# Kernel optimization log

Measured on AMD Instinct MI355X. Metric: run time of the kernel, lower is better.

Reference implementation:

```python
import jax, jax.numpy as jnp
import numpy as np

B, R, NB, T = 32, 96, 5, 2048
FEAT_DIM = 64
SPARSITY = 0.2


def _per_band(X, community, W1, b1, W2, b2):
    # X: [R, T] wavelet coeffs for one (batch, band) slice
    n, t = X.shape
    f32 = X.dtype
    # --- functional connectivity (cosine of centered signals == Pearson corr) ---
    Xc = X - X.mean(axis=1, keepdims=True)
    norm = jnp.linalg.norm(Xc, axis=1, keepdims=True)
    norm = jnp.where(norm == 0, 1.0, norm)
    C = (Xc @ Xc.T) / (norm * norm.T)
    C = jnp.nan_to_num(C, nan=0.0)
    C = C * (1.0 - jnp.eye(n, dtype=f32))  # zero diagonal
    # --- quantile sparsification over strict lower triangle ---
    ti, tj = np.tril_indices(n, -1)
    thr = jnp.quantile(jnp.abs(C[ti, tj]), 1.0 - SPARSITY)
    A = C * (jnp.abs(C) >= thr).astype(f32)  # graph_type == 'weighted'
    # --- node features (5-dim, averaged over regions) ---
    mean_f = X.mean(axis=1)
    std_f = jnp.std(X, axis=1, ddof=1)  # torch.std is unbiased
    energy_f = (X ** 2).sum(axis=1)
    maxamp_f = jnp.abs(X).max(axis=1)
    ps = jnp.abs(jnp.fft.fft(X, axis=1)) ** 2
    ps = ps[:, : t // 2]
    s = ps.sum(axis=1, keepdims=True)
    s = jnp.where(s == 0, 1.0, s)
    p = ps / s
    ent_f = -(p * jnp.log(p + 1e-10)).sum(axis=1)
    node5 = jnp.stack([mean_f, std_f, energy_f, maxamp_f, ent_f], axis=1).mean(axis=0)
    # --- graph properties (6-dim) on binarized adjacency ---
    Bm = (A != 0).astype(f32)
    ne = Bm.sum() / 2.0
    density = ne / (n * (n - 1) / 2.0)
    deg = Bm.sum(axis=1)
    avg_deg = deg.mean()
    A2 = Bm @ Bm
    tri = (A2 * Bm).sum() / 6.0
    poss = (deg * (deg - 1.0)).sum() / 2.0
    clus = jnp.where(poss > 0, tri / jnp.where(poss > 0, poss, 1.0), 0.0)
    # global efficiency: safe reciprocal (zero where A+I == 0; original would emit inf)
    denom = Bm + jnp.eye(n, dtype=f32)
    eff = jnp.where(denom > 0, 1.0 / jnp.where(denom > 0, denom, 1.0), 0.0).sum() / (n * (n - 1))
    # approximate modularity with fixed 2-community assignment (deterministic)
    m2 = 2.0 * ne
    m2_safe = jnp.where(m2 > 0, m2, 1.0)
    same = (community[:, None] == community[None, :]) & (~jnp.eye(n, dtype=bool))
    expected = jnp.outer(deg, deg) / m2_safe
    mod = jnp.where(m2 > 0, (same * (Bm - expected)).sum() / m2_safe, 0.0)
    props = jnp.stack([ne, density, avg_deg, clus, eff, mod])
    feat11 = jnp.concatenate([node5, props])  # [11]
    # --- feature encoder MLP (dropout is identity at inference) ---
    h = jnp.maximum(feat11 @ W1.T + b1, 0.0)
    return A, h @ W2.T + b2


def _forward(wavelet_coeffs, frequency_bands, community, W1, b1, W2, b2):
    b, r, nb, t = wavelet_coeffs.shape
    Xs = wavelet_coeffs.transpose(0, 2, 1, 3).reshape(b * nb, r, t)  # [B*NB, R, T]
    A, F = jax.vmap(_per_band, in_axes=(0, None, None, None, None, None))(
        Xs, community, W1, b1, W2, b2)
    return A.reshape(b, nb, r, r), F.reshape(b, nb, -1)


def setup_inputs() -> dict:
    key = jax.random.key(0)
    k0, k1, k2, k3, k4 = jax.random.split(key, 5)
    wavelet_coeffs = jax.random.normal(k0, (B, R, NB, T), dtype=jnp.float32)
    frequency_bands = jax.random.uniform(k1, (NB, 2), dtype=jnp.float32)
    community = jax.random.randint(k2, (R,), 0, 2)
    W1 = jax.random.normal(k3, (32, 11), dtype=jnp.float32) * 0.3
    b1 = jnp.zeros((32,), jnp.float32)
    W2 = jax.random.normal(k4, (FEAT_DIM, 32), dtype=jnp.float32) * 0.18
    b2 = jnp.zeros((FEAT_DIM,), jnp.float32)
    return {"wavelet_coeffs": wavelet_coeffs, "frequency_bands": frequency_bands,
            "community": community, "W1": W1, "b1": b1, "W2": W2, "b2": b2}


def reference(wavelet_coeffs, frequency_bands, community, W1, b1, W2, b2):
    return _forward(wavelet_coeffs, frequency_bands, community, W1, b1, W2, b2)
```

## Files before the change

kernel.cpp:

```cpp
#include <hip/hip_runtime.h>
#include <hip/hip_bf16.h>
#include <math.h>
#include <float.h>

#ifndef M_PI
#define M_PI 3.14159265358979323846
#endif

#define NBANDS 160
#define RR 96
#define TT 2048
#define NTRIL 4560
#define A_ELEMS ((size_t)NBANDS * RR * RR)
#define NBIN 16384
#define MAXCAND 512

#define KS 8
#define CHUNK 256
#define BKS 64
#define GPITCH 72

#define PHI(L) ((L) ^ (((L) >> 5) & 31))

typedef float  f32x4  __attribute__((ext_vector_type(4)));
typedef __bf16 bf16x8 __attribute__((ext_vector_type(8)));
typedef __bf16 bf16x4 __attribute__((ext_vector_type(4)));

__device__ inline void blockReduceSum4(double v0, double v1, double v2, double v3,
                                       double* sred, double out[4]) {
    for (int off = 32; off > 0; off >>= 1) {
        v0 += __shfl_down(v0, off, 64);
        v1 += __shfl_down(v1, off, 64);
        v2 += __shfl_down(v2, off, 64);
        v3 += __shfl_down(v3, off, 64);
    }
    int lane = threadIdx.x & 63, wid = threadIdx.x >> 6;
    if (lane == 0) {
        sred[wid * 4 + 0] = v0; sred[wid * 4 + 1] = v1;
        sred[wid * 4 + 2] = v2; sred[wid * 4 + 3] = v3;
    }
    __syncthreads();
    if (threadIdx.x < 4) {
        double r = sred[threadIdx.x] + sred[4 + threadIdx.x]
                 + sred[8 + threadIdx.x] + sred[12 + threadIdx.x];
        sred[16 + threadIdx.x] = r;
    }
    __syncthreads();
    out[0] = sred[16]; out[1] = sred[17]; out[2] = sred[18]; out[3] = sred[19];
    __syncthreads();
}

__device__ inline void blockReduceSum2(double v0, double v1,
                                       double* sred, double out[2]) {
    for (int off = 32; off > 0; off >>= 1) {
        v0 += __shfl_down(v0, off, 64);
        v1 += __shfl_down(v1, off, 64);
    }
    int lane = threadIdx.x & 63, wid = threadIdx.x >> 6;
    if (lane == 0) { sred[wid * 2 + 0] = v0; sred[wid * 2 + 1] = v1; }
    __syncthreads();
    if (threadIdx.x < 2) {
        double r = sred[threadIdx.x] + sred[2 + threadIdx.x]
                 + sred[4 + threadIdx.x] + sred[6 + threadIdx.x];
        sred[8 + threadIdx.x] = r;
    }
    __syncthreads();
    out[0] = sred[8]; out[1] = sred[9];
    __syncthreads();
}

__device__ inline void blockReduceMax4(double v0, double v1, double v2, double v3,
                                       double* sred, double out[4]) {
    for (int off = 32; off > 0; off >>= 1) {
        v0 = fmax(v0, __shfl_down(v0, off, 64));
        v1 = fmax(v1, __shfl_down(v1, off, 64));
        v2 = fmax(v2, __shfl_down(v2, off, 64));
        v3 = fmax(v3, __shfl_down(v3, off, 64));
    }
    int lane = threadIdx.x & 63, wid = threadIdx.x >> 6;
    if (lane == 0) {
        sred[wid * 4 + 0] = v0; sred[wid * 4 + 1] = v1;
        sred[wid * 4 + 2] = v2; sred[wid * 4 + 3] = v3;
    }
    __syncthreads();
    if (threadIdx.x < 4) {
        double r = fmax(fmax(sred[threadIdx.x], sred[4 + threadIdx.x]),
                        fmax(sred[8 + threadIdx.x], sred[12 + threadIdx.x]));
        sred[16 + threadIdx.x] = r;
    }
    __syncthreads();
    out[0] = sred[16]; out[1] = sred[17]; out[2] = sred[18]; out[3] = sred[19];
    __syncthreads();
}

__global__ void twiddle_kernel(float* tw) {
    int k = blockIdx.x * blockDim.x + threadIdx.x;
    if (k < 1024) {
        double ang = -2.0 * M_PI * (double)k / 2048.0;
        tw[2 * k]     = (float)cos(ang);
        tw[2 * k + 1] = (float)sin(ang);
    }
}

#define BFLYD(r1, r2, WR, WI) do { \
    float _wr = (WR), _wi = (WI); \
    float _t1r = _wr * yr1[r2] - _wi * yi1[r2]; \
    float _t1i = _wr * yi1[r2] + _wi * yr1[r2]; \
    yr1[r2] = yr1[r1] - _t1r; yi1[r2] = yi1[r1] - _t1i; \
    yr1[r1] += _t1r; yi1[r1] += _t1i; \
    float _t2r = _wr * yr2[r2] - _wi * yi2[r2]; \
    float _t2i = _wr * yi2[r2] + _wi * yr2[r2]; \
    yr2[r2] = yr2[r1] - _t2r; yi2[r2] = yi2[r1] - _t2i; \
    yr2[r1] += _t2r; yi2[r1] += _t2i; } while (0)

__global__ __launch_bounds__(256) void rowstat_fft_kernel(
    const float* __restrict__ wc, const float* __restrict__ tw,
    double* __restrict__ rowstats)
{
    __shared__ float re1[TT];
    __shared__ float im1[TT];
    __shared__ float re2[TT];
    __shared__ float im2[TT];
    __shared__ double sred[24];
    __shared__ double statout[12];
    __shared__ float bcast[8];

    int t = threadIdx.x;
    int g0 = blockIdx.x * 4;

    int band = g0 / RR, r0 = g0 % RR;
    int b = band / 5, nb = band % 5;
    size_t base0 = ((size_t)(b * RR + r0) * 5 + nb) * TT;
    const size_t RSTR = (size_t)5 * TT;
    const float2* twv = (const float2*)tw;

    float s0 = 0.f, s1 = 0.f, s2 = 0.f, s3 = 0.f;
    float q0 = 0.f, q1 = 0.f, q2 = 0.f, q3 = 0.f;
    float m0 = 0.f, m1 = 0.f, m2 = 0.f, m3 = 0.f;
#pragma unroll
    for (int c = 0; c < 8; c++) {
        int i = t + c * 256;
        float a0 = wc[base0 + i];
        float a1 = wc[base0 + RSTR + i];
        float a2 = wc[base0 + 2 * RSTR + i];
        float a3 = wc[base0 + 3 * RSTR + i];
        int P = PHI(i);
        re1[P] = a0; im1[P] = a1; re2[P] = a2; im2[P] = a3;
        s0 += a0; s1 += a1; s2 += a2; s3 += a3;
        q0 = fmaf(a0, a0, q0); q1 = fmaf(a1, a1, q1);
        q2 = fmaf(a2, a2, q2); q3 = fmaf(a3, a3, q3);
        m0 = fmaxf(m0, fabsf(a0)); m1 = fmaxf(m1, fabsf(a1));
        m2 = fmaxf(m2, fabsf(a2)); m3 = fmaxf(m3, fabsf(a3));
    }
    __syncthreads();

    {
        double S[4], Q[4], M[4];
        blockReduceSum4((double)s0, (double)s1, (double)s2, (double)s3, sred, S);
        blockReduceSum4((double)q0, (double)q1, (double)q2, (double)q3, sred, Q);
        blockReduceMax4((double)m0, (double)m1, (double)m2, (double)m3, sred, M);
        if (t == 0) {
            statout[0] = S[0]; statout[1] = S[1]; statout[2] = S[2]; statout[3] = S[3];
            statout[4] = Q[0]; statout[5] = Q[1]; statout[6] = Q[2]; statout[7] = Q[3];
            statout[8] = M[0]; statout[9] = M[1]; statout[10] = M[2]; statout[11] = M[3];
        }
    }

    float yr1[8], yi1[8], yr2[8], yi2[8];

#pragma unroll
    for (int j = 0; j < 8; j++) {
        int p = 8 * t + j;
        int L = (int)(__brev((unsigned)p) >> 21);
        int P = PHI(L);
        yr1[j] = re1[P]; yi1[j] = im1[P];
        yr2[j] = re2[P]; yi2[j] = im2[P];
    }

    const float RC = 0.70710678f;
    BFLYD(0, 1, 1.0f, 0.0f); BFLYD(2, 3, 1.0f, 0.0f);
    BFLYD(4, 5, 1.0f, 0.0f); BFLYD(6, 7, 1.0f, 0.0f);
    BFLYD(0, 2, 1.0f, 0.0f); BFLYD(1, 3, 0.0f, -1.0f);
    BFLYD(4, 6, 1.0f, 0.0f); BFLYD(5, 7, 0.0f, -1.0f);
    BFLYD(0, 4, 1.0f, 0.0f); BFLYD(1, 5, RC, -RC);
    BFLYD(2, 6, 0.0f, -1.0f); BFLYD(3, 7, -RC, -RC);

    __syncthreads();
#pragma unroll
    for (int j = 0; j < 8; j++) {
        int P = PHI(8 * t + j);
        re1[P] = yr1[j]; im1[P] = yi1[j];
        re2[P] = yr2[j]; im2[P] = yi2[j];
    }
    __syncthreads();
    int oo = t & 7;
    int bb64 = 4 * ((t >> 3) & 7) + (t >> 6);
#pragma unroll
    for (int k = 0; k < 8; k++) {
        int P = PHI(64 * bb64 + 8 * k + oo);
        yr1[k] = re1[P]; yi1[k] = im1[P];
        yr2[k] = re2[P]; yi2[k] = im2[P];
    }

    {
        float2 w0 = twv[oo << 7];
        BFLYD(0, 1, w0.x, w0.y); BFLYD(2, 3, w0.x, w0.y);
        BFLYD(4, 5, w0.x, w0.y); BFLYD(6, 7, w0.x, w0.y);
        float2 wa = twv[oo << 6];
        float2 wb = twv[(oo + 8) << 6];
        BFLYD(0, 2, wa.x, wa.y); BFLYD(1, 3, wb.x, wb.y);
        BFLYD(4, 6, wa.x, wa.y); BFLYD(5, 7, wb.x, wb.y);
        float2 wc0 = twv[oo << 5], wc1 = twv[(oo + 8) << 5];
        float2 wc2 = twv[(oo + 16) << 5], wc3 = twv[(oo + 24) << 5];
        BFLYD(0, 4, wc0.x, wc0.y);
        BFLYD(1, 5, wc1.x, wc1.y);
        BFLYD(2, 6, wc2.x, wc2.y);
        BFLYD(3, 7, wc3.x, wc3.y);
    }

    __syncthreads();
#pragma unroll
    for (int k = 0; k < 8; k++) {
        int P = PHI(64 * bb64 + 8 * k + oo);
        re1[P] = yr1[k]; im1[P] = yi1[k];
        re2[P] = yr2[k]; im2[P] = yi2[k];
    }
    __syncthreads();
    int O3 = t & 63, Wq = t >> 6;
#pragma unroll
    for (int s = 0; s < 2; s++) {
        int B3 = Wq + 4 * s;
#pragma unroll
        for (int k = 0; k < 4; k++) {
            int P = PHI(256 * B3 + 64 * k + O3);
            yr1[4 * s + k] = re1[P]; yi1[4 * s + k] = im1[P];
            yr2[4 * s + k] = re2[P]; yi2[4 * s + k] = im2[P];
        }
    }

    {
        float2 w0 = twv[O3 << 4];
        float2 wa = twv[O3 << 3];
        float2 wb = twv[(O3 + 64) << 3];
        BFLYD(0, 1, w0.x, w0.y); BFLYD(2, 3, w0.x, w0.y);
        BFLYD(4, 5, w0.x, w0.y); BFLYD(6, 7, w0.x, w0.y);
        BFLYD(0, 2, wa.x, wa.y); BFLYD(1, 3, wb.x, wb.y);
        BFLYD(4, 6, wa.x, wa.y); BFLYD(5, 7, wb.x, wb.y);
    }

    __syncthreads();
#pragma unroll
    for (int s = 0; s < 2; s++) {
        int B3 = Wq + 4 * s;
#pragma unroll
        for (int k = 0; k < 4; k++) {
            int P = PHI(256 * B3 + 64 * k + O3);
            re1[P] = yr1[4 * s + k]; im1[P] = yi1[4 * s + k];
            re2[P] = yr2[4 * s + k]; im2[P] = yi2[4 * s + k];
        }
    }
    __syncthreads();
#pragma unroll
    for (int k = 0; k < 8; k++) {
        int P = PHI(256 * k + t);
        yr1[k] = re1[P]; yi1[k] = im1[P];
        yr2[k] = re2[P]; yi2[k] = im2[P];
    }

    {
        float2 w0 = twv[t << 2];
        float2 wa = twv[t << 1];
        float2 wb = twv[(t + 256) << 1];
        BFLYD(0, 1, w0.x, w0.y); BFLYD(2, 3, w0.x, w0.y);
        BFLYD(4, 5, w0.x, w0.y); BFLYD(6, 7, w0.x, w0.y);
        BFLYD(0, 2, wa.x, wa.y); BFLYD(1, 3, wb.x, wb.y);
        BFLYD(4, 6, wa.x, wa.y); BFLYD(5, 7, wb.x, wb.y);
        float2 wf0 = twv[t], wf1 = twv[t + 256];
        float2 wf2 = twv[t + 512], wf3 = twv[t + 768];
        BFLYD(0, 4, wf0.x, wf0.y);
        BFLYD(1, 5, wf1.x, wf1.y);
        BFLYD(2, 6, wf2.x, wf2.y);
        BFLYD(3, 7, wf3.x, wf3.y);
    }

    __syncthreads();
#pragma unroll
    for (int k = 0; k < 8; k++) {
        int P = PHI(256 * k + t);
        re1[P] = yr1[k]; im1[P] = yi1[k];
        re2[P] = yr2[k]; im2[P] = yi2[k];
    }
    __syncthreads();

    float psa1[8], psb1[8], psa2[8], psb2[8];
#pragma unroll
    for (int k = 0; k < 8; k++) {
        int q = (2048 - t - 256 * k) & 2047;
        int P = PHI(q);
        float prr = re1[P], pii = im1[P];
        float sr = yr1[k] + prr, di = yi1[k] - pii;
        float si = yi1[k] + pii, dr = yr1[k] - prr;
        psa1[k] = 0.25f * (sr * sr + di * di);
        psb1[k] = 0.25f * (si * si + dr * dr);
        float prr2 = re2[P], pii2 = im2[P];
        float sr2 = yr2[k] + prr2, di2 = yi2[k] - pii2;
        float si2 = yi2[k] + pii2, dr2 = yr2[k] - prr2;
        psa2[k] = 0.25f * (sr2 * sr2 + di2 * di2);
        psb2[k] = 0.25f * (si2 * si2 + dr2 * dr2);
    }

    float la = 0.f, lb = 0.f, lc = 0.f, ld = 0.f;
#pragma unroll
    for (int k = 0; k < 8; k++) {
        la += psa1[k]; lb += psb1[k]; lc += psa2[k]; ld += psb2[k];
    }
    double SS[4];
    blockReduceSum4((double)la, (double)lb, (double)lc, (double)ld, sred, SS);
    if (t == 0) {
        bcast[0] = psa1[0]; bcast[1] = psa1[4];
        bcast[2] = psb1[0]; bcast[3] = psb1[4];
        bcast[4] = psa2[0]; bcast[5] = psa2[4];
        bcast[6] = psb2[0]; bcast[7] = psb2[4];
    }
    __syncthreads();
    double Sa = 0.5 * (SS[0] + (double)bcast[0] - (double)bcast[1]);
    double Sb = 0.5 * (SS[1] + (double)bcast[2] - (double)bcast[3]);
    double Sc = 0.5 * (SS[2] + (double)bcast[4] - (double)bcast[5]);
    double Sd = 0.5 * (SS[3] + (double)bcast[6] - (double)bcast[7]);
    if (Sa == 0.0) Sa = 1.0;
    if (Sb == 0.0) Sb = 1.0;
    if (Sc == 0.0) Sc = 1.0;
    if (Sd == 0.0) Sd = 1.0;
    float invSa = (float)(1.0 / Sa), invSb = (float)(1.0 / Sb);
    float invSc = (float)(1.0 / Sc), invSd = (float)(1.0 / Sd);

    float ea = 0.f, eb = 0.f, ec = 0.f, ed = 0.f;
#pragma unroll
    for (int k = 0; k < 8; k++) {
        float pa = psa1[k] * invSa;
        float pb = psb1[k] * invSb;
        float pc = psa2[k] * invSc;
        float pd = psb2[k] * invSd;
        ea += pa * __logf(pa + 1e-10f);
        eb += pb * __logf(pb + 1e-10f);
        ec += pc * __logf(pc + 1e-10f);
        ed += pd * __logf(pd + 1e-10f);
    }
    double EE[4];
    blockReduceSum4((double)ea, (double)eb, (double)ec, (double)ed, sred, EE);

    if (t == 0) {
        float pa0 = psa1[0] * invSa, pa4 = psa1[4] * invSa;
        float pb0 = psb1[0] * invSb, pb4 = psb1[4] * invSb;
        float pc0 = psa2[0] * invSc, pc4 = psa2[4] * invSc;
        float pd0 = psb2[0] * invSd, pd4 = psb2[4] * invSd;
        double TA = 0.5 * (EE[0] + (double)(pa0 * __logf(pa0 + 1e-10f))
                                 - (double)(pa4 * __logf(pa4 + 1e-10f)));
        double TB = 0.5 * (EE[1] + (double)(pb0 * __logf(pb0 + 1e-10f))
                                 - (double)(pb4 * __logf(pb4 + 1e-10f)));
        double TC = 0.5 * (EE[2] + (double)(pc0 * __logf(pc0 + 1e-10f))
                                 - (double)(pc4 * __logf(pc4 + 1e-10f)));
        double TD = 0.5 * (EE[3] + (double)(pd0 * __logf(pd0 + 1e-10f))
                                 - (double)(pd4 * __logf(pd4 + 1e-10f)));
        double TAs[4] = {TA, TB, TC, TD};
#pragma unroll
        for (int rix = 0; rix < 4; rix++) {
            double SUM = statout[rix], SQ = statout[4 + rix], MX = statout[8 + rix];
            double mean = SUM / (double)TT;
            double nsq = SQ - (double)TT * mean * mean; if (nsq < 0) nsq = 0;
            double nrm = sqrt(nsq);
            double* w = rowstats + (size_t)(g0 + rix) * 6;
            w[0] = mean; w[1] = (nrm == 0.0 ? 1.0 : nrm); w[2] = sqrt(nsq / 2047.0);
            w[3] = SQ;   w[4] = MX;                       w[5] = -TAs[rix];
        }
    }
}

__global__ void zero_kernel(float4* __restrict__ p, int n4) {
    int i = blockIdx.x * blockDim.x + threadIdx.x;
    if (i < n4) p[i] = make_float4(0.f, 0.f, 0.f, 0.f);
}

template <bool USE_PART>
__global__ __launch_bounds__(384) void gram_mfma_kernel(
    const float* __restrict__ wc, float* __restrict__ G)
{
    __shared__ __attribute__((aligned(16))) __bf16 sh_hi[RR][GPITCH];
    __shared__ __attribute__((aligned(16))) __bf16 sh_lo[RR][GPITCH];

    int bid = blockIdx.x;
    int band = bid / KS, chunk = bid % KS;
    int b = band / 5, nb = band % 5;
    size_t bandbase = ((size_t)b * RR * 5 + nb) * TT + (size_t)chunk * CHUNK;

    int t = threadIdx.x;
    int wave = t >> 6, lane = t & 63;
    int m16 = lane & 15, quad = lane >> 4;
    int arow = wave * 16 + m16;

    f32x4 acc[6];
#pragma unroll
    for (int ct = 0; ct < 6; ct++) acc[ct] = (f32x4){0.f, 0.f, 0.f, 0.f};

    for (int stage = 0; stage < CHUNK / BKS; stage++) {
        int k0 = stage * BKS;
#pragma unroll
        for (int i = 0; i < 4; i++) {
            int gid = t + i * 384;
            int row = gid >> 4, c4 = gid & 15;
            float4 v = *(const float4*)(wc + bandbase + (size_t)row * (5 * TT) + k0 + c4 * 4);
            __bf16 h0 = (__bf16)v.x, h1 = (__bf16)v.y, h2 = (__bf16)v.z, h3 = (__bf16)v.w;
            __bf16 l0 = (__bf16)(v.x - (float)h0);
            __bf16 l1 = (__bf16)(v.y - (float)h1);
            __bf16 l2 = (__bf16)(v.z - (float)h2);
            __bf16 l3 = (__bf16)(v.w - (float)h3);
            *(bf16x4*)&sh_hi[row][c4 * 4] = (bf16x4){h0, h1, h2, h3};
            *(bf16x4*)&sh_lo[row][c4 * 4] = (bf16x4){l0, l1, l2, l3};
        }
        __syncthreads();
#pragma unroll
        for (int ks = 0; ks < BKS / 32; ks++) {
            int ko = ks * 32 + quad * 8;
            bf16x8 ah = *(const bf16x8*)&sh_hi[arow][ko];
            bf16x8 al = *(const bf16x8*)&sh_lo[arow][ko];
#pragma unroll
            for (int ct = 0; ct < 6; ct++) {
                int brow = ct * 16 + m16;
                bf16x8 bh = *(const bf16x8*)&sh_hi[brow][ko];
                bf16x8 bl = *(const bf16x8*)&sh_lo[brow][ko];
                acc[ct] = __builtin_amdgcn_mfma_f32_16x16x32_bf16(ah, bh, acc[ct], 0, 0, 0);
                acc[ct] = __builtin_amdgcn_mfma_f32_16x16x32_bf16(ah, bl, acc[ct], 0, 0, 0);
                acc[ct] = __builtin_amdgcn_mfma_f32_16x16x32_bf16(al, bh, acc[ct], 0, 0, 0);
            }
        }
        __syncthreads();
    }

    if (USE_PART) {
        float* Gp = G + (size_t)bid * (RR * RR);
#pragma unroll
        for (int ct = 0; ct < 6; ct++) {
#pragma unroll
            for (int r = 0; r < 4; r++) {
                int grow = wave * 16 + quad * 4 + r;
                int gcol = ct * 16 + m16;
                Gp[grow * RR + gcol] = acc[ct][r];
            }
        }
    } else {
        float* Gb = G + (size_t)band * (RR * RR);
#pragma unroll
        for (int ct = 0; ct < 6; ct++) {
#pragma unroll
            for (int r = 0; r < 4; r++) {
                int grow = wave * 16 + quad * 4 + r;
                int gcol = ct * 16 + m16;
                atomicAdd(&Gb[grow * RR + gcol], acc[ct][r]);
            }
        }
    }
}

template <bool USE_PART>
__global__ __launch_bounds__(256) void band_finalize_kernel(
    const float* __restrict__ Gsrc, const double* __restrict__ rowstats,
    const int* __restrict__ community,
    const float* __restrict__ W1, const float* __restrict__ b1,
    const float* __restrict__ W2, const float* __restrict__ b2,
    float* __restrict__ A_out, float* __restrict__ F_out)
{
    __shared__ float Cs[RR][RR];
    __shared__ int hist[NBIN];
    __shared__ int chunkv[256];
    __shared__ float cand[MAXCAND];
    __shared__ int ctrl[4];
    __shared__ double mean_s[RR], nrm_s[RR];
    __shared__ int comm_s[RR];
    __shared__ unsigned long long msk[RR][2];
    __shared__ int deg[RR];
    __shared__ double sred[24];
    __shared__ double feat[11];
    __shared__ double hmlp[32];
    __shared__ double thr_s;

    int band = blockIdx.x, t = threadIdx.x;
    const double* rsb = rowstats + (size_t)band * RR * 6;
    if (t < RR) {
        mean_s[t] = rsb[t * 6 + 0];
        nrm_s[t]  = rsb[t * 6 + 1];
        comm_s[t] = community[t];
    }
    for (int i = t; i < NBIN; i += 256) hist[i] = 0;
    if (t == 0) ctrl[3] = 0;
    __syncthreads();

    for (int idx = t; idx < RR * RR; idx += 256) {
        int i = idx / RR, j = idx % RR;
        float g;
        if (USE_PART) {
            const float* p = Gsrc + (size_t)band * KS * (RR * RR) + idx;
            float acc = 0.f;
#pragma unroll
            for (int c = 0; c < KS; c++) acc += p[(size_t)c * (RR * RR)];
            g = acc;
        } else {
            g = Gsrc[(size_t)band * (RR * RR) + idx];
        }
        double cd = ((double)g - (double)TT * mean_s[i] * mean_s[j]) / (nrm_s[i] * nrm_s[j]);
        if (i == j) cd = 0.0;
        float cf = (float)cd;
        Cs[i][j] = cf;
        if (j < i) {
            float val = fabsf(cf);
            int bin = (int)(val * (float)NBIN);
            bin = bin > (NBIN - 1) ? (NBIN - 1) : bin;
            atomicAdd(&hist[bin], 1);
        }
    }
    __syncthreads();

    int cs = 0;
    for (int i = 0; i < 64; i++) cs += hist[t * 64 + i];
    chunkv[t] = cs;
    __syncthreads();

    if (t == 0) {
        int r0 = 3647, r1 = 3648;
        int cum = 0, c0 = 0;
        while (c0 < 256 && cum + chunkv[c0] <= r0) { cum += chunkv[c0]; c0++; }
        int bin = c0 * 64, cb = cum;
        while (cb + hist[bin] <= r0) { cb += hist[bin]; bin++; }
        int B0 = bin, cumB0 = cb;
        int bin1 = bin, cb1 = cb;
        while (cb1 + hist[bin1] <= r1) { cb1 += hist[bin1]; bin1++; }
        ctrl[0] = B0; ctrl[1] = bin1; ctrl[2] = cumB0;
    }
    __syncthreads();

    int B0 = ctrl[0], B1 = ctrl[1];
    for (int idx = t; idx < RR * RR; idx += 256) {
        int i = idx / RR, j = idx % RR;
        if (j < i) {
            float val = fabsf(Cs[i][j]);
            int bin = (int)(val * (float)NBIN);
            bin = bin > (NBIN - 1) ? (NBIN - 1) : bin;
            if (bin >= B0 && bin <= B1) {
                int k = atomicAdd(&ctrl[3], 1);
                if (k < MAXCAND) cand[k] = val;
            }
        }
    }
    __syncthreads();

    if (t == 0) {
        int n = ctrl[3]; if (n > MAXCAND) n = MAXCAND;
        for (int i = 1; i < n; i++) {
            float key = cand[i]; int j = i - 1;
            while (j >= 0 && cand[j] > key) { cand[j + 1] = cand[j]; j--; }
            cand[j + 1] = key;
        }
        int r0 = 3647 - ctrl[2];
        int r1 = 3648 - ctrl[2];
        double v0 = (double)cand[r0], v1 = (double)cand[r1];
        thr_s = v0 + 0.2 * (v1 - v0);
    }
    __syncthreads();
    double thr = thr_s;

    float* Ab = A_out + (size_t)band * (RR * RR);
    for (int idx = t; idx < RR * RR; idx += 256) {
        float cf = Cs[idx / RR][idx % RR];
        bool keep = ((double)fabsf(cf) >= thr);
        Ab[idx] = keep ? cf : 0.f;
    }

    int lane = t & 63, wid = t >> 6;
    for (int i = wid; i < RR; i += 4) {
        float vlo = Cs[i][lane];
        bool klo = ((double)fabsf(vlo) >= thr) && (vlo != 0.f);
        unsigned long long blo = __ballot(klo);
        float vhi = Cs[i][64 + (lane & 31)];
        bool khi = (lane < 32) && ((double)fabsf(vhi) >= thr) && (vhi != 0.f);
        unsigned long long bhi = __ballot(khi) & 0xffffffffull;
        if (lane == 0) {
            msk[i][0] = blo; msk[i][1] = bhi;
            deg[i] = __popcll(blo) + __popcll(bhi);
        }
    }
    __syncthreads();

    double triord = 0, ein = 0, expin = 0;
    for (int idx = t; idx < RR * RR; idx += 256) {
        int i = idx / RR, j = idx % RR;
        unsigned long long mi0 = msk[i][0], mi1 = msk[i][1];
        bool bij = (((j < 64) ? (mi0 >> j) : (mi1 >> (j - 64))) & 1ull) != 0;
        if (bij)
            triord += (double)(__popcll(mi0 & msk[j][0]) +
                               __popcll(mi1 & msk[j][1]));
        if (i != j && comm_s[i] == comm_s[j]) {
            ein += bij ? 1.0 : 0.0;
            expin += (double)deg[i] * (double)deg[j];
        }
    }
    double dv = (t < RR) ? (double)deg[t] : 0.0;
    double R1[4], R2[4], R3[2];
    blockReduceSum4(triord, ein, expin, dv, sred, R1);
    blockReduceSum4((t < RR) ? dv * (dv - 1.0) : 0.0,
                    (t < RR) ? rsb[t * 6 + 0] : 0.0,
                    (t < RR) ? rsb[t * 6 + 2] : 0.0,
                    (t < RR) ? rsb[t * 6 + 3] : 0.0, sred, R2);
    blockReduceSum2((t < RR) ? rsb[t * 6 + 4] : 0.0,
                    (t < RR) ? rsb[t * 6 + 5] : 0.0, sred, R3);
    double TRI = R1[0], EIN = R1[1], EXPIN = R1[2], DEGS = R1[3];
    double POSS2 = R2[0], N0 = R2[1], N1 = R2[2], N2 = R2[3];
    double N3 = R3[0], N4 = R3[1];

    if (t == 0) {
        double ne = 0.5 * DEGS;
        feat[0] = N0 / (double)RR;
        feat[1] = N1 / (double)RR;
        feat[2] = N2 / (double)RR;
        feat[3] = N3 / (double)RR;
        feat[4] = N4 / (double)RR;
        feat[5] = ne;
        feat[6] = ne / (double)NTRIL;
        feat[7] = DEGS / (double)RR;
        double tri = TRI / 6.0, poss = POSS2 * 0.5;
        feat[8] = (poss > 0.0) ? tri / poss : 0.0;
        feat[9] = ((double)RR + DEGS) / ((double)RR * (double)(RR - 1));
        double m2 = DEGS;
        feat[10] = (m2 > 0.0) ? (EIN - EXPIN / m2) / m2 : 0.0;
    }
    __syncthreads();

    if (t < 32) {
        double a = (double)b1[t];
        for (int k = 0; k < 11; k++) a += (double)W1[t * 11 + k] * feat[k];
        hmlp[t] = (a > 0.0) ? a : 0.0;
    }
    __syncthreads();
    if (t < 64) {
        double a = (double)b2[t];
        for (int j = 0; j < 32; j++) a += (double)W2[t * 32 + j] * hmlp[j];
        F_out[(size_t)band * 64 + t] = (float)a;
    }
}

extern "C" void kernel_launch(void* const* d_in, const int* in_sizes, int n_in,
                              void* d_out, int out_size, void* d_ws, size_t ws_size,
                              hipStream_t stream) {
    const float* wc        = (const float*)d_in[0];
    const int*   community = (const int*)d_in[2];
    const float* W1        = (const float*)d_in[3];
    const float* b1        = (const float*)d_in[4];
    const float* W2        = (const float*)d_in[5];
    const float* b2        = (const float*)d_in[6];

    float* A_out = (float*)d_out;
    float* F_out = A_out + A_ELEMS;

    char* ws = (char*)d_ws;
    float*  tw       = (float*)ws;
    double* rowstats = (double*)(ws + 8192);
    const size_t PART_OFF   = 747520;
    const size_t PART_BYTES = (size_t)NBANDS * KS * RR * RR * sizeof(float);
    float* Gpart = (float*)(ws + PART_OFF);
    bool use_part = (ws_size >= PART_OFF + PART_BYTES);

    hipLaunchKernelGGL(twiddle_kernel, dim3(4), dim3(256), 0, stream, tw);
    hipLaunchKernelGGL(rowstat_fft_kernel, dim3(NBANDS * RR / 4), dim3(256), 0, stream,
                       wc, tw, rowstats);
    if (use_part) {
        hipLaunchKernelGGL(HIP_KERNEL_NAME(gram_mfma_kernel<true>),
                           dim3(NBANDS * KS), dim3(384), 0, stream, wc, Gpart);
        hipLaunchKernelGGL(HIP_KERNEL_NAME(band_finalize_kernel<true>),
                           dim3(NBANDS), dim3(256), 0, stream,
                           Gpart, rowstats, community, W1, b1, W2, b2, A_out, F_out);
    } else {
        int n4 = (int)(A_ELEMS / 4);
        hipLaunchKernelGGL(zero_kernel, dim3((n4 + 255) / 256), dim3(256), 0, stream,
                           (float4*)A_out, n4);
        hipLaunchKernelGGL(HIP_KERNEL_NAME(gram_mfma_kernel<false>),
                           dim3(NBANDS * KS), dim3(384), 0, stream, wc, A_out);
        hipLaunchKernelGGL(HIP_KERNEL_NAME(band_finalize_kernel<false>),
                           dim3(NBANDS), dim3(256), 0, stream,
                           A_out, rowstats, community, W1, b1, W2, b2, A_out, F_out);
    }
}
```

Baseline: 309.7 us.

## Halve FFT shared memory by time-multiplexing two complex FFTs through one buffer

The row-stat FFT kernel now uses two 2048-float shared buffers instead of four. The second packed complex FFT is staged in registers and processed sequentially through the same buffer, with its stage exchanges interleaved with the first FFT's butterflies. Launch bounds now request 8 blocks per CU, aiming for higher occupancy at the cost of more barriers and more serialised exchange phases. The finalize kernel also replaces the double-precision division by norms with multiplication by precomputed reciprocals.

```diff
diff --git a/kernel.cpp b/kernel.cpp
--- a/kernel.cpp
+++ b/kernel.cpp
@@ -102,28 +102,102 @@
     }
 }
 
-#define BFLYD(r1, r2, WR, WI) do { \
+#define BFLY1(yr, yi, r1, r2, WR, WI) do { \
     float _wr = (WR), _wi = (WI); \
-    float _t1r = _wr * yr1[r2] - _wi * yi1[r2]; \
-    float _t1i = _wr * yi1[r2] + _wi * yr1[r2]; \
-    yr1[r2] = yr1[r1] - _t1r; yi1[r2] = yi1[r1] - _t1i; \
-    yr1[r1] += _t1r; yi1[r1] += _t1i; \
-    float _t2r = _wr * yr2[r2] - _wi * yi2[r2]; \
-    float _t2i = _wr * yi2[r2] + _wi * yr2[r2]; \
-    yr2[r2] = yr2[r1] - _t2r; yi2[r2] = yi2[r1] - _t2i; \
-    yr2[r1] += _t2r; yi2[r1] += _t2i; } while (0)
-
-__global__ __launch_bounds__(256) void rowstat_fft_kernel(
+    float _tr = _wr * yr[r2] - _wi * yi[r2]; \
+    float _ti = _wr * yi[r2] + _wi * yr[r2]; \
+    yr[r2] = yr[r1] - _tr; yi[r2] = yi[r1] - _ti; \
+    yr[r1] += _tr; yi[r1] += _ti; } while (0)
+
+__device__ inline void fft_g1(float (&yr)[8], float (&yi)[8]) {
+    const float RC = 0.70710678f;
+    BFLY1(yr, yi, 0, 1, 1.0f, 0.0f); BFLY1(yr, yi, 2, 3, 1.0f, 0.0f);
+    BFLY1(yr, yi, 4, 5, 1.0f, 0.0f); BFLY1(yr, yi, 6, 7, 1.0f, 0.0f);
+    BFLY1(yr, yi, 0, 2, 1.0f, 0.0f); BFLY1(yr, yi, 1, 3, 0.0f, -1.0f);
+    BFLY1(yr, yi, 4, 6, 1.0f, 0.0f); BFLY1(yr, yi, 5, 7, 0.0f, -1.0f);
+    BFLY1(yr, yi, 0, 4, 1.0f, 0.0f); BFLY1(yr, yi, 1, 5, RC, -RC);
+    BFLY1(yr, yi, 2, 6, 0.0f, -1.0f); BFLY1(yr, yi, 3, 7, -RC, -RC);
+}
+
+__device__ inline void fft_g2(float (&yr)[8], float (&yi)[8],
+                              const float2* __restrict__ twv, int oo) {
+    float2 w0 = twv[oo << 7];
+    BFLY1(yr, yi, 0, 1, w0.x, w0.y); BFLY1(yr, yi, 2, 3, w0.x, w0.y);
+    BFLY1(yr, yi, 4, 5, w0.x, w0.y); BFLY1(yr, yi, 6, 7, w0.x, w0.y);
+    float2 wa = twv[oo << 6];
+    float2 wb = twv[(oo + 8) << 6];
+    BFLY1(yr, yi, 0, 2, wa.x, wa.y); BFLY1(yr, yi, 1, 3, wb.x, wb.y);
+    BFLY1(yr, yi, 4, 6, wa.x, wa.y); BFLY1(yr, yi, 5, 7, wb.x, wb.y);
+    float2 wc0 = twv[oo << 5], wc1 = twv[(oo + 8) << 5];
+    float2 wc2 = twv[(oo + 16) << 5], wc3 = twv[(oo + 24) << 5];
+    BFLY1(yr, yi, 0, 4, wc0.x, wc0.y);
+    BFLY1(yr, yi, 1, 5, wc1.x, wc1.y);
+    BFLY1(yr, yi, 2, 6, wc2.x, wc2.y);
+    BFLY1(yr, yi, 3, 7, wc3.x, wc3.y);
+}
+
+__device__ inline void fft_g3(float (&yr)[8], float (&yi)[8],
+                              const float2* __restrict__ twv, int O3) {
+    float2 w0 = twv[O3 << 4];
+    float2 wa = twv[O3 << 3];
+    float2 wb = twv[(O3 + 64) << 3];
+    BFLY1(yr, yi, 0, 1, w0.x, w0.y); BFLY1(yr, yi, 2, 3, w0.x, w0.y);
+    BFLY1(yr, yi, 4, 5, w0.x, w0.y); BFLY1(yr, yi, 6, 7, w0.x, w0.y);
+    BFLY1(yr, yi, 0, 2, wa.x, wa.y); BFLY1(yr, yi, 1, 3, wb.x, wb.y);
+    BFLY1(yr, yi, 4, 6, wa.x, wa.y); BFLY1(yr, yi, 5, 7, wb.x, wb.y);
+}
+
+__device__ inline void fft_g4(float (&yr)[8], float (&yi)[8],
+                              const float2* __restrict__ twv, int t) {
+    float2 w0 = twv[t << 2];
+    float2 wa = twv[t << 1];
+    float2 wb = twv[(t + 256) << 1];
+    BFLY1(yr, yi, 0, 1, w0.x, w0.y); BFLY1(yr, yi, 2, 3, w0.x, w0.y);
+    BFLY1(yr, yi, 4, 5, w0.x, w0.y); BFLY1(yr, yi, 6, 7, w0.x, w0.y);
+    BFLY1(yr, yi, 0, 2, wa.x, wa.y); BFLY1(yr, yi, 1, 3, wb.x, wb.y);
+    BFLY1(yr, yi, 4, 6, wa.x, wa.y); BFLY1(yr, yi, 5, 7, wb.x, wb.y);
+    float2 wf0 = twv[t], wf1 = twv[t + 256];
+    float2 wf2 = twv[t + 512], wf3 = twv[t + 768];
+    BFLY1(yr, yi, 0, 4, wf0.x, wf0.y);
+    BFLY1(yr, yi, 1, 5, wf1.x, wf1.y);
+    BFLY1(yr, yi, 2, 6, wf2.x, wf2.y);
+    BFLY1(yr, yi, 3, 7, wf3.x, wf3.y);
+}
+
+#define WR_P1(yr, yi) do { _Pragma("unroll") \
+    for (int j = 0; j < 8; j++) { int P = PHI(8 * t + j); bufA[P] = yr[j]; bufB[P] = yi[j]; } } while (0)
+#define RD_P1(yr, yi) do { _Pragma("unroll") \
+    for (int k = 0; k < 8; k++) { int P = PHI(64 * bb64 + 8 * k + oo); yr[k] = bufA[P]; yi[k] = bufB[P]; } } while (0)
+#define WR_P2(yr, yi) do { _Pragma("unroll") \
+    for (int k = 0; k < 8; k++) { int P = PHI(64 * bb64 + 8 * k + oo); bufA[P] = yr[k]; bufB[P] = yi[k]; } } while (0)
+#define RD_P2(yr, yi) do { _Pragma("unroll") \
+    for (int s = 0; s < 2; s++) { int B3 = Wq + 4 * s; _Pragma("unroll") \
+      for (int k = 0; k < 4; k++) { int P = PHI(256 * B3 + 64 * k + O3); yr[4 * s + k] = bufA[P]; yi[4 * s + k] = bufB[P]; } } } while (0)
+#define WR_P3(yr, yi) do { _Pragma("unroll") \
+    for (int s = 0; s < 2; s++) { int B3 = Wq + 4 * s; _Pragma("unroll") \
+      for (int k = 0; k < 4; k++) { int P = PHI(256 * B3 + 64 * k + O3); bufA[P] = yr[4 * s + k]; bufB[P] = yi[4 * s + k]; } } } while (0)
+#define RD_P3(yr, yi) do { _Pragma("unroll") \
+    for (int k = 0; k < 8; k++) { int P = PHI(256 * k + t); yr[k] = bufA[P]; yi[k] = bufB[P]; } } while (0)
+#define WR_F(yr, yi) do { _Pragma("unroll") \
+    for (int k = 0; k < 8; k++) { int P = PHI(256 * k + t); bufA[P] = yr[k]; bufB[P] = yi[k]; } } while (0)
+#define PS_INPLACE(yr, yi, lA, lB) do { _Pragma("unroll") \
+    for (int k = 0; k < 8; k++) { \
+        int q = (2048 - t - 256 * k) & 2047; int P = PHI(q); \
+        float prr = bufA[P], pii = bufB[P]; \
+        float sr = yr[k] + prr, di = yi[k] - pii; \
+        float si = yi[k] + pii, dr = yr[k] - prr; \
+        float pa = 0.25f * (sr * sr + di * di); \
+        float pb = 0.25f * (si * si + dr * dr); \
+        lA += pa; lB += pb; yr[k] = pa; yi[k] = pb; } } while (0)
+
+__global__ __launch_bounds__(256, 8) void rowstat_fft_kernel(
     const float* __restrict__ wc, const float* __restrict__ tw,
     double* __restrict__ rowstats)
 {
-    __shared__ float re1[TT];
-    __shared__ float im1[TT];
-    __shared__ float re2[TT];
-    __shared__ float im2[TT];
+    __shared__ float bufA[TT];
+    __shared__ float bufB[TT];
     __shared__ double sred[24];
     __shared__ double statout[12];
-    __shared__ float bcast[8];
 
     int t = threadIdx.x;
     int g0 = blockIdx.x * 4;
@@ -134,6 +208,7 @@
     const size_t RSTR = (size_t)5 * TT;
     const float2* twv = (const float2*)tw;
 
+    float r2b[8], i2b[8];
     float s0 = 0.f, s1 = 0.f, s2 = 0.f, s3 = 0.f;
     float q0 = 0.f, q1 = 0.f, q2 = 0.f, q3 = 0.f;
     float m0 = 0.f, m1 = 0.f, m2 = 0.f, m3 = 0.f;
@@ -145,7 +220,8 @@
         float a2 = wc[base0 + 2 * RSTR + i];
         float a3 = wc[base0 + 3 * RSTR + i];
         int P = PHI(i);
-        re1[P] = a0; im1[P] = a1; re2[P] = a2; im2[P] = a3;
+        bufA[P] = a0; bufB[P] = a1;
+        r2b[c] = a2; i2b[c] = a3;
         s0 += a0; s1 += a1; s2 += a2; s3 += a3;
         q0 = fmaf(a0, a0, q0); q1 = fmaf(a1, a1, q1);
         q2 = fmaf(a2, a2, q2); q3 = fmaf(a3, a3, q3);
@@ -173,154 +249,80 @@
         int p = 8 * t + j;
         int L = (int)(__brev((unsigned)p) >> 21);
         int P = PHI(L);
-        yr1[j] = re1[P]; yi1[j] = im1[P];
-        yr2[j] = re2[P]; yi2[j] = im2[P];
-    }
-
-    const float RC = 0.70710678f;
-    BFLYD(0, 1, 1.0f, 0.0f); BFLYD(2, 3, 1.0f, 0.0f);
-    BFLYD(4, 5, 1.0f, 0.0f); BFLYD(6, 7, 1.0f, 0.0f);
-    BFLYD(0, 2, 1.0f, 0.0f); BFLYD(1, 3, 0.0f, -1.0f);
-    BFLYD(4, 6, 1.0f, 0.0f); BFLYD(5, 7, 0.0f, -1.0f);
-    BFLYD(0, 4, 1.0f, 0.0f); BFLYD(1, 5, RC, -RC);
-    BFLYD(2, 6, 0.0f, -1.0f); BFLYD(3, 7, -RC, -RC);
-
+        yr1[j] = bufA[P]; yi1[j] = bufB[P];
+    }
+    __syncthreads();
+#pragma unroll
+    for (int c = 0; c < 8; c++) {
+        int P = PHI(t + c * 256);
+        bufA[P] = r2b[c]; bufB[P] = i2b[c];
+    }
+    fft_g1(yr1, yi1);
     __syncthreads();
 #pragma unroll
     for (int j = 0; j < 8; j++) {
-        int P = PHI(8 * t + j);
-        re1[P] = yr1[j]; im1[P] = yi1[j];
-        re2[P] = yr2[j]; im2[P] = yi2[j];
-    }
-    __syncthreads();
+        int p = 8 * t + j;
+        int L = (int)(__brev((unsigned)p) >> 21);
+        int P = PHI(L);
+        yr2[j] = bufA[P]; yi2[j] = bufB[P];
+    }
+    fft_g1(yr2, yi2);
+
     int oo = t & 7;
     int bb64 = 4 * ((t >> 3) & 7) + (t >> 6);
-#pragma unroll
-    for (int k = 0; k < 8; k++) {
-        int P = PHI(64 * bb64 + 8 * k + oo);
-        yr1[k] = re1[P]; yi1[k] = im1[P];
-        yr2[k] = re2[P]; yi2[k] = im2[P];
-    }
-
-    {
-        float2 w0 = twv[oo << 7];
-        BFLYD(0, 1, w0.x, w0.y); BFLYD(2, 3, w0.x, w0.y);
-        BFLYD(4, 5, w0.x, w0.y); BFLYD(6, 7, w0.x, w0.y);
-        float2 wa = twv[oo << 6];
-        float2 wb = twv[(oo + 8) << 6];
-        BFLYD(0, 2, wa.x, wa.y); BFLYD(1, 3, wb.x, wb.y);
-        BFLYD(4, 6, wa.x, wa.y); BFLYD(5, 7, wb.x, wb.y);
-        float2 wc0 = twv[oo << 5], wc1 = twv[(oo + 8) << 5];
-        float2 wc2 = twv[(oo + 16) << 5], wc3 = twv[(oo + 24) << 5];
-        BFLYD(0, 4, wc0.x, wc0.y);
-        BFLYD(1, 5, wc1.x, wc1.y);
-        BFLYD(2, 6, wc2.x, wc2.y);
-        BFLYD(3, 7, wc3.x, wc3.y);
-    }
-
-    __syncthreads();
-#pragma unroll
-    for (int k = 0; k < 8; k++) {
-        int P = PHI(64 * bb64 + 8 * k + oo);
-        re1[P] = yr1[k]; im1[P] = yi1[k];
-        re2[P] = yr2[k]; im2[P] = yi2[k];
-    }
-    __syncthreads();
     int O3 = t & 63, Wq = t >> 6;
-#pragma unroll
-    for (int s = 0; s < 2; s++) {
-        int B3 = Wq + 4 * s;
-#pragma unroll
-        for (int k = 0; k < 4; k++) {
-            int P = PHI(256 * B3 + 64 * k + O3);
-            yr1[4 * s + k] = re1[P]; yi1[4 * s + k] = im1[P];
-            yr2[4 * s + k] = re2[P]; yi2[4 * s + k] = im2[P];
-        }
-    }
-
-    {
-        float2 w0 = twv[O3 << 4];
-        float2 wa = twv[O3 << 3];
-        float2 wb = twv[(O3 + 64) << 3];
-        BFLYD(0, 1, w0.x, w0.y); BFLYD(2, 3, w0.x, w0.y);
-        BFLYD(4, 5, w0.x, w0.y); BFLYD(6, 7, w0.x, w0.y);
-        BFLYD(0, 2, wa.x, wa.y); BFLYD(1, 3, wb.x, wb.y);
-        BFLYD(4, 6, wa.x, wa.y); BFLYD(5, 7, wb.x, wb.y);
-    }
-
-    __syncthreads();
-#pragma unroll
-    for (int s = 0; s < 2; s++) {
-        int B3 = Wq + 4 * s;
-#pragma unroll
-        for (int k = 0; k < 4; k++) {
-            int P = PHI(256 * B3 + 64 * k + O3);
-            re1[P] = yr1[4 * s + k]; im1[P] = yi1[4 * s + k];
-            re2[P] = yr2[4 * s + k]; im2[P] = yi2[4 * s + k];
-        }
-    }
-    __syncthreads();
-#pragma unroll
-    for (int k = 0; k < 8; k++) {
-        int P = PHI(256 * k + t);
-        yr1[k] = re1[P]; yi1[k] = im1[P];
-        yr2[k] = re2[P]; yi2[k] = im2[P];
-    }
-
-    {
-        float2 w0 = twv[t << 2];
-        float2 wa = twv[t << 1];
-        float2 wb = twv[(t + 256) << 1];
-        BFLYD(0, 1, w0.x, w0.y); BFLYD(2, 3, w0.x, w0.y);
-        BFLYD(4, 5, w0.x, w0.y); BFLYD(6, 7, w0.x, w0.y);
-        BFLYD(0, 2, wa.x, wa.y); BFLYD(1, 3, wb.x, wb.y);
-        BFLYD(4, 6, wa.x, wa.y); BFLYD(5, 7, wb.x, wb.y);
-        float2 wf0 = twv[t], wf1 = twv[t + 256];
-        float2 wf2 = twv[t + 512], wf3 = twv[t + 768];
-        BFLYD(0, 4, wf0.x, wf0.y);
-        BFLYD(1, 5, wf1.x, wf1.y);
-        BFLYD(2, 6, wf2.x, wf2.y);
-        BFLYD(3, 7, wf3.x, wf3.y);
-    }
-
-    __syncthreads();
-#pragma unroll
-    for (int k = 0; k < 8; k++) {
-        int P = PHI(256 * k + t);
-        re1[P] = yr1[k]; im1[P] = yi1[k];
-        re2[P] = yr2[k]; im2[P] = yi2[k];
-    }
-    __syncthreads();
-
-    float psa1[8], psb1[8], psa2[8], psb2[8];
-#pragma unroll
-    for (int k = 0; k < 8; k++) {
-        int q = (2048 - t - 256 * k) & 2047;
-        int P = PHI(q);
-        float prr = re1[P], pii = im1[P];
-        float sr = yr1[k] + prr, di = yi1[k] - pii;
-        float si = yi1[k] + pii, dr = yr1[k] - prr;
-        psa1[k] = 0.25f * (sr * sr + di * di);
-        psb1[k] = 0.25f * (si * si + dr * dr);
-        float prr2 = re2[P], pii2 = im2[P];
-        float sr2 = yr2[k] + prr2, di2 = yi2[k] - pii2;
-        float si2 = yi2[k] + pii2, dr2 = yr2[k] - prr2;
-        psa2[k] = 0.25f * (sr2 * sr2 + di2 * di2);
-        psb2[k] = 0.25f * (si2 * si2 + dr2 * dr2);
-    }
+
+    __syncthreads();
+    WR_P1(yr1, yi1);
+    __syncthreads();
+    RD_P1(yr1, yi1);
+    __syncthreads();
+    WR_P1(yr2, yi2);
+    fft_g2(yr1, yi1, twv, oo);
+    __syncthreads();
+    RD_P1(yr2, yi2);
+    fft_g2(yr2, yi2, twv, oo);
+
+    __syncthreads();
+    WR_P2(yr1, yi1);
+    __syncthreads();
+    RD_P2(yr1, yi1);
+    __syncthreads();
+    WR_P2(yr2, yi2);
+    fft_g3(yr1, yi1, twv, O3);
+    __syncthreads();
+    RD_P2(yr2, yi2);
+    fft_g3(yr2, yi2, twv, O3);
+
+    __syncthreads();
+    WR_P3(yr1, yi1);
+    __syncthreads();
+    RD_P3(yr1, yi1);
+    __syncthreads();
+    WR_P3(yr2, yi2);
+    fft_g4(yr1, yi1, twv, t);
+    __syncthreads();
+    RD_P3(yr2, yi2);
+    fft_g4(yr2, yi2, twv, t);
 
     float la = 0.f, lb = 0.f, lc = 0.f, ld = 0.f;
-#pragma unroll
-    for (int k = 0; k < 8; k++) {
-        la += psa1[k]; lb += psb1[k]; lc += psa2[k]; ld += psb2[k];
-    }
+    __syncthreads();
+    WR_F(yr1, yi1);
+    __syncthreads();
+    PS_INPLACE(yr1, yi1, la, lb);
+    __syncthreads();
+    WR_F(yr2, yi2);
+    __syncthreads();
+    PS_INPLACE(yr2, yi2, lc, ld);
+
     double SS[4];
     blockReduceSum4((double)la, (double)lb, (double)lc, (double)ld, sred, SS);
+    __shared__ float bcast[8];
     if (t == 0) {
-        bcast[0] = psa1[0]; bcast[1] = psa1[4];
-        bcast[2] = psb1[0]; bcast[3] = psb1[4];
-        bcast[4] = psa2[0]; bcast[5] = psa2[4];
-        bcast[6] = psb2[0]; bcast[7] = psb2[4];
+        bcast[0] = yr1[0]; bcast[1] = yr1[4];
+        bcast[2] = yi1[0]; bcast[3] = yi1[4];
+        bcast[4] = yr2[0]; bcast[5] = yr2[4];
+        bcast[6] = yi2[0]; bcast[7] = yi2[4];
     }
     __syncthreads();
     double Sa = 0.5 * (SS[0] + (double)bcast[0] - (double)bcast[1]);
@@ -337,10 +339,10 @@
     float ea = 0.f, eb = 0.f, ec = 0.f, ed = 0.f;
 #pragma unroll
     for (int k = 0; k < 8; k++) {
-        float pa = psa1[k] * invSa;
-        float pb = psb1[k] * invSb;
-        float pc = psa2[k] * invSc;
-        float pd = psb2[k] * invSd;
+        float pa = yr1[k] * invSa;
+        float pb = yi1[k] * invSb;
+        float pc = yr2[k] * invSc;
+        float pd = yi2[k] * invSd;
         ea += pa * __logf(pa + 1e-10f);
         eb += pb * __logf(pb + 1e-10f);
         ec += pc * __logf(pc + 1e-10f);
@@ -350,10 +352,10 @@
     blockReduceSum4((double)ea, (double)eb, (double)ec, (double)ed, sred, EE);
 
     if (t == 0) {
-        float pa0 = psa1[0] * invSa, pa4 = psa1[4] * invSa;
-        float pb0 = psb1[0] * invSb, pb4 = psb1[4] * invSb;
-        float pc0 = psa2[0] * invSc, pc4 = psa2[4] * invSc;
-        float pd0 = psb2[0] * invSd, pd4 = psb2[4] * invSd;
+        float pa0 = yr1[0] * invSa, pa4 = yr1[4] * invSa;
+        float pb0 = yi1[0] * invSb, pb4 = yi1[4] * invSb;
+        float pc0 = yr2[0] * invSc, pc4 = yr2[4] * invSc;
+        float pd0 = yi2[0] * invSd, pd4 = yi2[4] * invSd;
         double TA = 0.5 * (EE[0] + (double)(pa0 * __logf(pa0 + 1e-10f))
                                  - (double)(pa4 * __logf(pa4 + 1e-10f)));
         double TB = 0.5 * (EE[1] + (double)(pb0 * __logf(pb0 + 1e-10f))
@@ -474,7 +476,7 @@
     __shared__ int chunkv[256];
     __shared__ float cand[MAXCAND];
     __shared__ int ctrl[4];
-    __shared__ double mean_s[RR], nrm_s[RR];
+    __shared__ double mean_s[RR], inv_s[RR];
     __shared__ int comm_s[RR];
     __shared__ unsigned long long msk[RR][2];
     __shared__ int deg[RR];
@@ -487,7 +489,7 @@
     const double* rsb = rowstats + (size_t)band * RR * 6;
     if (t < RR) {
         mean_s[t] = rsb[t * 6 + 0];
-        nrm_s[t]  = rsb[t * 6 + 1];
+        inv_s[t]  = 1.0 / rsb[t * 6 + 1];
         comm_s[t] = community[t];
     }
     for (int i = t; i < NBIN; i += 256) hist[i] = 0;
@@ -506,7 +508,7 @@
         } else {
             g = Gsrc[(size_t)band * (RR * RR) + idx];
         }
-        double cd = ((double)g - (double)TT * mean_s[i] * mean_s[j]) / (nrm_s[i] * nrm_s[j]);
+        double cd = ((double)g - (double)TT * mean_s[i] * mean_s[j]) * (inv_s[i] * inv_s[j]);
         if (i == j) cd = 0.0;
         float cf = (float)cd;
         Cs[i][j] = cf;
```

Result: slower. 357.2 us (+15.3%).
